# Kernel tuning notes

Hardware: AMD Instinct MI355X
Metric: run time of the kernel (lower is better)

Reference implementation:

```python
import jax, jax.numpy as jnp
import numpy as np

N_E, FEAT, REST = 2048, 512, 8
HEAD, LENGTH = 8, 64


def setup_inputs() -> dict:
    key = jax.random.key(0)
    kx, kq, kk, kd = jax.random.split(key, 4)
    x = jax.random.normal(kx, (N_E, FEAT, REST), dtype=jnp.float32)
    Q = jax.random.normal(kq, (HEAD, LENGTH, FEAT), dtype=jnp.float32)
    K = jax.random.normal(kk, (HEAD, LENGTH, FEAT), dtype=jnp.float32)
    D = jax.random.normal(kd, (HEAD, LENGTH, FEAT), dtype=jnp.float32)
    return {"x": x, "Q": Q, "K": K, "D": D}


def _linear(a, W):
    # a: (n, f, *rest), W: (h, q, f) -> y: (n, h, q, *rest)
    y = jnp.einsum('nf...,hqf->nhq...', a, W)
    # L2-normalize over the last 3 axes (here: h? no -- axes (q, rest...) per the
    # original code: sum over (-1,-2,-3) of (n,h,q,rest) = (h,q,rest) per n)
    norm = jnp.sqrt((y * y).sum((-1, -2, -3), keepdims=True))
    return y / norm


def reference(x, Q, K, D):
    n_e = x.shape[0]
    rest = x.shape[2:]
    head, length = Q.shape[0], Q.shape[1]
    q = _linear(x, Q)  # (n, h, l, rest)
    k = _linear(x, K)
    d = _linear(x, D)
    # scores over electrons: contract (l, rest) -> (h, n, n)
    w = jax.nn.softmax(jnp.einsum('nh...,mh...->hnm', q, k), axis=-1)
    # weighted combine: (h,n,m) x (m,h,l,rest) -> (n,h,l,rest)
    v = jnp.einsum('hnm,mhl...->nhl...', w, d)
    return v.reshape((n_e, head * length) + rest)
```

## Files before the change

kernel.cpp:

```cpp
#include <hip/hip_runtime.h>
#include <math.h>

#define NE   2048
#define FEAT 512

typedef short short8 __attribute__((ext_vector_type(8)));
typedef float f32x4  __attribute__((ext_vector_type(4)));

__device__ __forceinline__ unsigned short f2bf(float f) {
    union { float f; unsigned u; } v; v.f = f;
    unsigned r = v.u + 0x7fffu + ((v.u >> 16) & 1u);
    return (unsigned short)(r >> 16);
}
__device__ __forceinline__ float bf2f(unsigned b) {
    union { unsigned u; float f; } v; v.u = b << 16;
    return v.f;
}
__device__ __forceinline__ unsigned pack2(float a, float b) {
    return (unsigned)f2bf(a) | ((unsigned)f2bf(b) << 16);
}

__device__ __forceinline__ void gld16(unsigned short* lds, const unsigned short* g) {
    __builtin_amdgcn_global_load_lds(
        (const __attribute__((address_space(1))) unsigned int*)g,
        (__attribute__((address_space(3))) unsigned int*)lds,
        16, 0, 0);
}


__global__ __launch_bounds__(256) void wconv_kernel(
    const float* __restrict__ Wq, const float* __restrict__ Wk, const float* __restrict__ Wd,
    unsigned short* __restrict__ wbf)
{
    const int t = threadIdx.x;
    const float* W = (blockIdx.y == 0) ? Wq : (blockIdx.y == 1) ? Wk : Wd;
    unsigned short* o = wbf + (size_t)blockIdx.y * 262144;
    const int idx = blockIdx.x * 2048 + t * 8;
    const float4* p = (const float4*)(W + idx);
    float4 v0 = p[0], v1 = p[1];
    *(uint4*)(o + idx) = make_uint4(pack2(v0.x, v0.y), pack2(v0.z, v0.w),
                                    pack2(v1.x, v1.y), pack2(v1.z, v1.w));
}

__global__ __launch_bounds__(256) void xpose_kernel(const float* __restrict__ x,
                                                    unsigned short* __restrict__ xt)
{
    __shared__ float xs[8 * 516];
    const int t = threadIdx.x;
    const int n = blockIdx.x;
    const float4* xp = (const float4*)(x + (size_t)n * 4096);
    #pragma unroll
    for (int i = 0; i < 4; ++i) {
        int idx = t + 256 * i;
        float4 v = xp[idx];
        int f = idx >> 1, rh = (idx & 1) * 4;
        xs[(rh + 0) * 516 + f] = v.x;
        xs[(rh + 1) * 516 + f] = v.y;
        xs[(rh + 2) * 516 + f] = v.z;
        xs[(rh + 3) * 516 + f] = v.w;
    }
    __syncthreads();
    const int r = t >> 5, f0 = (t & 31) * 16;
    const float* src = &xs[r * 516 + f0];
    unsigned o[8];
    #pragma unroll
    for (int j = 0; j < 8; ++j) o[j] = pack2(src[2 * j], src[2 * j + 1]);
    unsigned short* dst = xt + (size_t)n * 4096 + r * 512 + f0;
    *(uint4*)dst       = make_uint4(o[0], o[1], o[2], o[3]);
    *(uint4*)(dst + 8) = make_uint4(o[4], o[5], o[6], o[7]);
}

__global__ __launch_bounds__(256) void proj_gemm(
    const unsigned short* __restrict__ wbf, const unsigned short* __restrict__ xt,
    unsigned short* __restrict__ qb, unsigned short* __restrict__ kb, unsigned short* __restrict__ db)
{
    __shared__ unsigned short SM[17408];
    const int t = threadIdx.x;
    const int w = blockIdx.z;
    const unsigned short* W = wbf + (size_t)w * 262144;
    unsigned short* out = (w == 0) ? qb : (w == 1) ? kb : db;
    const int M0 = blockIdx.y * 128;
    const int N0 = blockIdx.x * 128;
    const int wave = t >> 6, lane = t & 63, quad = lane >> 4, l16 = lane & 15;
    const int lrow = lane >> 3;
    const int scol = ((lane & 7) ^ lrow) * 8;
    unsigned short* As = SM;
    unsigned short* Bs = SM + 8192;

    f32x4 acc[2][8];
    #pragma unroll
    for (int i = 0; i < 2; ++i)
        #pragma unroll
        for (int j = 0; j < 8; ++j) acc[i][j] = {0.f, 0.f, 0.f, 0.f};

    for (int kc = 0; kc < 8; ++kc) {
        #pragma unroll
        for (int p = 0; p < 4; ++p) {
            int c = p * 4 + wave;
            gld16(As + c * 512, W  + (size_t)(M0 + c * 8 + lrow) * 512 + kc * 64 + scol);
            gld16(Bs + c * 512, xt + (size_t)(N0 + c * 8 + lrow) * 512 + kc * 64 + scol);
        }
        __syncthreads();
        #pragma unroll
        for (int kk = 0; kk < 2; ++kk) {
            int so = ((kk * 4 + quad) ^ (l16 & 7)) * 8;
            short8 a0 = *(const short8*)&As[(wave * 32 + l16) * 64 + so];
            short8 a1 = *(const short8*)&As[(wave * 32 + 16 + l16) * 64 + so];
            #pragma unroll
            for (int ct = 0; ct < 8; ++ct) {
                short8 bb = *(const short8*)&Bs[(ct * 16 + l16) * 64 + so];
                acc[0][ct] = __builtin_amdgcn_mfma_f32_16x16x32_bf16(a0, bb, acc[0][ct], 0, 0, 0);
                acc[1][ct] = __builtin_amdgcn_mfma_f32_16x16x32_bf16(a1, bb, acc[1][ct], 0, 0, 0);
            }
        }
        __syncthreads();
    }

    unsigned short* T = SM;
    #pragma unroll
    for (int rt = 0; rt < 2; ++rt)
        #pragma unroll
        for (int reg = 0; reg < 4; ++reg) {
            int row = wave * 32 + rt * 16 + quad * 4 + reg;
            #pragma unroll
            for (int ct = 0; ct < 8; ++ct)
                T[row * 136 + ct * 16 + l16] = f2bf(acc[rt][ct][reg]);
        }
    __syncthreads();
    #pragma unroll
    for (int i = 0; i < 8; ++i) {
        int c = t + 256 * i;
        int n = c >> 7, row = c & 127;
        uint4 v = *(const uint4*)(T + row * 136 + n * 8);
        int hl = M0 + row;
        unsigned short* dst = out + (size_t)(hl >> 6) * 1048576 + (size_t)(hl & 63) * 8
                                  + (size_t)((N0 >> 3) + n) * 512;
        *(uint4*)dst = v;
    }
}

__global__ __launch_bounds__(256) void scales_kernel(
    const unsigned short* __restrict__ qb, const unsigned short* __restrict__ kb,
    const unsigned short* __restrict__ db, float* __restrict__ scales)
{
    __shared__ float red[256];
    const int t = threadIdx.x;
    const int n = blockIdx.x, w = blockIdx.y;
    const unsigned short* src = (w == 0) ? qb : (w == 1) ? kb : db;
    const int h = t >> 5, f0 = (t & 31) * 16;
    const unsigned short* p = src + ((size_t)h * NE + n) * 512 + f0;
    uint4 v0 = *(const uint4*)p;
    uint4 v1 = *(const uint4*)(p + 8);
    unsigned a[8] = {v0.x, v0.y, v0.z, v0.w, v1.x, v1.y, v1.z, v1.w};
    float s = 0.f;
    #pragma unroll
    for (int j = 0; j < 8; ++j) {
        float lo = bf2f(a[j] & 0xffffu), hi = bf2f(a[j] >> 16);
        s += lo * lo + hi * hi;
    }
    red[t] = s;
    __syncthreads();
    for (int st = 128; st > 0; st >>= 1) {
        if (t < st) red[t] += red[t + st];
        __syncthreads();
    }
    if (t == 0) scales[w * NE + n] = rsqrtf(red[0]);
}

__global__ __launch_bounds__(256) void dtrans_kernel(
    const unsigned short* __restrict__ db, const float* __restrict__ invd,
    unsigned short* __restrict__ dT)
{
    __shared__ float Ts[64 * 68];
    const int t = threadIdx.x;
    const int h = blockIdx.z, n0 = blockIdx.y * 64, f0 = blockIdx.x * 64;
    const int rr = t >> 3, cs = (t & 7) * 8;
    #pragma unroll
    for (int p = 0; p < 2; ++p) {
        int row = rr + p * 32;
        float sc = invd[n0 + row];
        uint4 v = *(const uint4*)(db + ((size_t)h * NE + n0 + row) * 512 + f0 + cs);
        unsigned a[4] = {v.x, v.y, v.z, v.w};
        float* d = &Ts[row * 68 + cs];
        #pragma unroll
        for (int j = 0; j < 4; ++j) {
            d[2 * j]     = bf2f(a[j] & 0xffffu) * sc;
            d[2 * j + 1] = bf2f(a[j] >> 16) * sc;
        }
    }
    __syncthreads();
    const int f = t >> 2, ns = (t & 3) * 16;
    unsigned o[8];
    #pragma unroll
    for (int j = 0; j < 8; ++j)
        o[j] = pack2(Ts[(ns + 2 * j) * 68 + f], Ts[(ns + 2 * j + 1) * 68 + f]);
    unsigned short* dst = dT + ((size_t)h * 512 + f0 + f) * NE + n0 + ns;
    *(uint4*)dst       = make_uint4(o[0], o[1], o[2], o[3]);
    *(uint4*)(dst + 8) = make_uint4(o[4], o[5], o[6], o[7]);
}

__global__ __launch_bounds__(256) void score_kernel(
    const unsigned short* __restrict__ qb, const unsigned short* __restrict__ kb,
    const float* __restrict__ scales, unsigned short* __restrict__ P,
    float* __restrict__ sums, int g)
{
    __shared__ unsigned short As[8192];
    __shared__ unsigned short Bs[8192];
    const int t = threadIdx.x;
    int bid = blockIdx.x + 16 * (blockIdx.y + 16 * blockIdx.z);
    int swz = (bid & 7) * 128 + (bid >> 3);
    const int bx = swz & 15, by = (swz >> 4) & 15, bz = swz >> 8;
    const int hg = bz, h = g * 4 + hg;
    const int n0 = by * 128, m0 = bx * 128;
    const int wave = t >> 6, lane = t & 63, quad = lane >> 4, l16 = lane & 15;
    const int lrow = lane >> 3;
    const int scol = ((lane & 7) ^ lrow) * 8;
    const unsigned short* qh = qb + (size_t)h * NE * 512;
    const unsigned short* kh = kb + (size_t)h * NE * 512;

    f32x4 acc[2][8];
    #pragma unroll
    for (int i = 0; i < 2; ++i)
        #pragma unroll
        for (int j = 0; j < 8; ++j) acc[i][j] = {0.f, 0.f, 0.f, 0.f};

    for (int kc = 0; kc < 8; ++kc) {
        #pragma unroll
        for (int p = 0; p < 4; ++p) {
            int c = p * 4 + wave;
            gld16(As + c * 512, qh + (size_t)(n0 + c * 8 + lrow) * 512 + kc * 64 + scol);
            gld16(Bs + c * 512, kh + (size_t)(m0 + c * 8 + lrow) * 512 + kc * 64 + scol);
        }
        __syncthreads();
        #pragma unroll
        for (int kk = 0; kk < 2; ++kk) {
            int so = ((kk * 4 + quad) ^ (l16 & 7)) * 8;
            short8 a0 = *(const short8*)&As[(wave * 32 + l16) * 64 + so];
            short8 a1 = *(const short8*)&As[(wave * 32 + 16 + l16) * 64 + so];
            #pragma unroll
            for (int ct = 0; ct < 8; ++ct) {
                short8 bb = *(const short8*)&Bs[(ct * 16 + l16) * 64 + so];
                acc[0][ct] = __builtin_amdgcn_mfma_f32_16x16x32_bf16(a0, bb, acc[0][ct], 0, 0, 0);
                acc[1][ct] = __builtin_amdgcn_mfma_f32_16x16x32_bf16(a1, bb, acc[1][ct], 0, 0, 0);
            }
        }
        __syncthreads();
    }

    float iq[2][4], ik[8];
    #pragma unroll
    for (int rt = 0; rt < 2; ++rt)
        #pragma unroll
        for (int reg = 0; reg < 4; ++reg)
            iq[rt][reg] = scales[n0 + wave * 32 + rt * 16 + quad * 4 + reg];
    #pragma unroll
    for (int ct = 0; ct < 8; ++ct) ik[ct] = scales[NE + m0 + ct * 16 + l16];

    unsigned short* Ph = P + (size_t)hg * NE * NE;
    #pragma unroll
    for (int rt = 0; rt < 2; ++rt)
        #pragma unroll
        for (int reg = 0; reg < 4; ++reg) {
            int nl = wave * 32 + rt * 16 + quad * 4 + reg;
            unsigned short* prow = Ph + (size_t)(n0 + nl) * NE + m0;
            float qs = iq[rt][reg];
            float rs = 0.f;
            #pragma unroll
            for (int ct = 0; ct < 8; ++ct) {
                float e = __expf(acc[rt][ct][reg] * qs * ik[ct]);
                unsigned short bx16 = f2bf(e);
                prow[ct * 16 + l16] = bx16;
                rs += bf2f(bx16);
            }
            rs += __shfl_xor(rs, 1);
            rs += __shfl_xor(rs, 2);
            rs += __shfl_xor(rs, 4);
            rs += __shfl_xor(rs, 8);
            if (l16 == 0) atomicAdd(&sums[hg * NE + n0 + nl], rs);
        }
}

__global__ __launch_bounds__(512) void combine_kernel(
    const unsigned short* __restrict__ P, const unsigned short* __restrict__ dT,
    const float* __restrict__ sums, float* __restrict__ out, int g)
{
    __shared__ unsigned short Ps[8192];
    __shared__ unsigned short Ds[8192];
    const int t = threadIdx.x;
    int bid = blockIdx.x + 4 * (blockIdx.y + 16 * blockIdx.z);
    int swz = (bid & 7) * 32 + (bid >> 3);
    const int bx = swz & 3, by = (swz >> 2) & 15, bz = swz >> 6;
    const int hg = bz, h = g * 4 + hg;
    const int n0 = by * 128, f0 = bx * 128;
    const int wave = t >> 6, lane = t & 63, quad = lane >> 4, l16 = lane & 15;
    const int wn = wave >> 1, wf = wave & 1;
    const int lrow = lane >> 3;
    const int scol = ((lane & 7) ^ lrow) * 8;
    const unsigned short* Ph = P + (size_t)hg * NE * NE;
    const unsigned short* dh = dT + (size_t)h * 512 * NE;

    f32x4 acc[2][4];
    #pragma unroll
    for (int i = 0; i < 2; ++i)
        #pragma unroll
        for (int j = 0; j < 4; ++j) acc[i][j] = {0.f, 0.f, 0.f, 0.f};

    for (int mc = 0; mc < 32; ++mc) {
        #pragma unroll
        for (int p = 0; p < 2; ++p) {
            int c = p * 8 + wave;
            gld16(Ps + c * 512, Ph + (size_t)(n0 + c * 8 + lrow) * NE + mc * 64 + scol);
            gld16(Ds + c * 512, dh + (size_t)(f0 + c * 8 + lrow) * NE + mc * 64 + scol);
        }
        __syncthreads();
        #pragma unroll
        for (int kk = 0; kk < 2; ++kk) {
            int so = ((kk * 4 + quad) ^ (l16 & 7)) * 8;
            short8 a0 = *(const short8*)&Ps[(wn * 32 + l16) * 64 + so];
            short8 a1 = *(const short8*)&Ps[(wn * 32 + 16 + l16) * 64 + so];
            #pragma unroll
            for (int ct = 0; ct < 4; ++ct) {
                short8 bb = *(const short8*)&Ds[(wf * 64 + ct * 16 + l16) * 64 + so];
                acc[0][ct] = __builtin_amdgcn_mfma_f32_16x16x32_bf16(a0, bb, acc[0][ct], 0, 0, 0);
                acc[1][ct] = __builtin_amdgcn_mfma_f32_16x16x32_bf16(a1, bb, acc[1][ct], 0, 0, 0);
            }
        }
        __syncthreads();
    }

    #pragma unroll
    for (int rt = 0; rt < 2; ++rt)
        #pragma unroll
        for (int reg = 0; reg < 4; ++reg) {
            int nl = wn * 32 + rt * 16 + quad * 4 + reg;
            float li = 1.0f / sums[hg * NE + n0 + nl];
            float* orow = out + (size_t)(n0 + nl) * 4096 + h * 512 + f0 + wf * 64;
            #pragma unroll
            for (int ct = 0; ct < 4; ++ct)
                orow[ct * 16 + l16] = acc[rt][ct][reg] * li;
        }
}

extern "C" void kernel_launch(void* const* d_in, const int* in_sizes, int n_in,
                              void* d_out, int out_size, void* d_ws, size_t ws_size,
                              hipStream_t stream)
{
    const float* x  = (const float*)d_in[0];
    const float* Qw = (const float*)d_in[1];
    const float* Kw = (const float*)d_in[2];
    const float* Dw = (const float*)d_in[3];
    float* out = (float*)d_out;

    char* ws = (char*)d_ws;
    unsigned short* xt = (unsigned short*)ws;
    unsigned short* db = (unsigned short*)(ws + 16777216);
    unsigned short* P  = (unsigned short*)ws;
    unsigned short* qb = (unsigned short*)(ws + 33554432);
    unsigned short* kb = (unsigned short*)(ws + 33554432 + 16777216);
    unsigned short* dT = (unsigned short*)(ws + 33554432 + 2 * 16777216);
    unsigned short* wbf = dT;
    float* scales = (float*)(ws + 83886080);
    float* sums   = (float*)(ws + 83886080 + 24576);

    wconv_kernel<<<dim3(128, 3), 256, 0, stream>>>(Qw, Kw, Dw, wbf);
    xpose_kernel<<<2048, 256, 0, stream>>>(x, xt);
    proj_gemm<<<dim3(128, 4, 3), 256, 0, stream>>>(wbf, xt, qb, kb, db);
    scales_kernel<<<dim3(2048, 3), 256, 0, stream>>>(qb, kb, db, scales);
    dtrans_kernel<<<dim3(8, 32, 8), 256, 0, stream>>>(db, scales + 2 * NE, dT);
    for (int g = 0; g < 2; ++g) {
        hipMemsetAsync(sums, 0, 4 * NE * sizeof(float), stream);
        score_kernel<<<dim3(16, 16, 4), 256, 0, stream>>>(qb, kb, scales, P, sums, g);
        combine_kernel<<<dim3(4, 16, 4), 512, 0, stream>>>(P, dT, sums, out, g);
    }
}
```

Baseline: 271.1 us.

## Double-buffer LDS loads in score and combine kernels, enlarge score tiles

The score kernel moves from 128x128 tiles with 256 threads to 256x256 tiles with 512 threads. It uses a two-stage LDS double buffer with explicit vmcnt waits and raw barriers, so global-to-LDS loads for step k+2 overlap compute on step k. The combine kernel gets the same double-buffered prefetch scheme. Larger tiles raise data reuse per loaded byte, but use 128KB of LDS and many accumulator registers per block, which lowers occupancy and leaves fewer blocks (256) to fill the CUs.

```diff
diff --git a/kernel.cpp b/kernel.cpp
--- a/kernel.cpp
+++ b/kernel.cpp
@@ -26,6 +26,13 @@
         (__attribute__((address_space(3))) unsigned int*)lds,
         16, 0, 0);
 }
+
+__device__ __forceinline__ void bar() {
+    asm volatile("" ::: "memory");
+    __builtin_amdgcn_s_barrier();
+    asm volatile("" ::: "memory");
+}
+#define VMW(n) asm volatile("s_waitcnt vmcnt(" #n ")" ::: "memory")
 
 
 __global__ __launch_bounds__(256) void wconv_kernel(
@@ -199,84 +206,101 @@
     *(uint4*)(dst + 8) = make_uint4(o[4], o[5], o[6], o[7]);
 }
 
-__global__ __launch_bounds__(256) void score_kernel(
+__global__ __launch_bounds__(512, 2) void score_kernel(
     const unsigned short* __restrict__ qb, const unsigned short* __restrict__ kb,
     const float* __restrict__ scales, unsigned short* __restrict__ P,
     float* __restrict__ sums, int g)
 {
-    __shared__ unsigned short As[8192];
-    __shared__ unsigned short Bs[8192];
-    const int t = threadIdx.x;
-    int bid = blockIdx.x + 16 * (blockIdx.y + 16 * blockIdx.z);
-    int swz = (bid & 7) * 128 + (bid >> 3);
-    const int bx = swz & 15, by = (swz >> 4) & 15, bz = swz >> 8;
+    __shared__ unsigned short SM[65536];
+    const int t = threadIdx.x;
+    int bid = blockIdx.x + 8 * (blockIdx.y + 8 * blockIdx.z);
+    int swz = (bid & 7) * 32 + (bid >> 3);
+    const int bx = swz & 7, by = (swz >> 3) & 7, bz = swz >> 6;
     const int hg = bz, h = g * 4 + hg;
-    const int n0 = by * 128, m0 = bx * 128;
+    const int n0 = by * 256, m0 = bx * 256;
     const int wave = t >> 6, lane = t & 63, quad = lane >> 4, l16 = lane & 15;
+    const int wr = wave >> 2, wc = wave & 3;
     const int lrow = lane >> 3;
     const int scol = ((lane & 7) ^ lrow) * 8;
     const unsigned short* qh = qb + (size_t)h * NE * 512;
     const unsigned short* kh = kb + (size_t)h * NE * 512;
 
-    f32x4 acc[2][8];
-    #pragma unroll
-    for (int i = 0; i < 2; ++i)
-        #pragma unroll
-        for (int j = 0; j < 8; ++j) acc[i][j] = {0.f, 0.f, 0.f, 0.f};
-
-    for (int kc = 0; kc < 8; ++kc) {
+    f32x4 acc[8][4];
+    #pragma unroll
+    for (int m = 0; m < 8; ++m)
+        #pragma unroll
+        for (int n = 0; n < 4; ++n) acc[m][n] = {0.f, 0.f, 0.f, 0.f};
+
+    auto STAGE = [&](int kc, int buf) {
+        unsigned short* A = SM + buf * 16384;
+        unsigned short* B = SM + 32768 + buf * 16384;
         #pragma unroll
         for (int p = 0; p < 4; ++p) {
-            int c = p * 4 + wave;
-            gld16(As + c * 512, qh + (size_t)(n0 + c * 8 + lrow) * 512 + kc * 64 + scol);
-            gld16(Bs + c * 512, kh + (size_t)(m0 + c * 8 + lrow) * 512 + kc * 64 + scol);
-        }
-        __syncthreads();
+            int c = p * 8 + wave;
+            gld16(A + c * 512, qh + (size_t)(n0 + c * 8 + lrow) * 512 + kc * 64 + scol);
+        }
+        #pragma unroll
+        for (int p = 0; p < 4; ++p) {
+            int c = p * 8 + wave;
+            gld16(B + c * 512, kh + (size_t)(m0 + c * 8 + lrow) * 512 + kc * 64 + scol);
+        }
+    };
+    auto COMPUTE = [&](int buf) {
+        const unsigned short* A = SM + buf * 16384;
+        const unsigned short* B = SM + 32768 + buf * 16384;
         #pragma unroll
         for (int kk = 0; kk < 2; ++kk) {
             int so = ((kk * 4 + quad) ^ (l16 & 7)) * 8;
-            short8 a0 = *(const short8*)&As[(wave * 32 + l16) * 64 + so];
-            short8 a1 = *(const short8*)&As[(wave * 32 + 16 + l16) * 64 + so];
-            #pragma unroll
-            for (int ct = 0; ct < 8; ++ct) {
-                short8 bb = *(const short8*)&Bs[(ct * 16 + l16) * 64 + so];
-                acc[0][ct] = __builtin_amdgcn_mfma_f32_16x16x32_bf16(a0, bb, acc[0][ct], 0, 0, 0);
-                acc[1][ct] = __builtin_amdgcn_mfma_f32_16x16x32_bf16(a1, bb, acc[1][ct], 0, 0, 0);
-            }
-        }
-        __syncthreads();
-    }
-
-    float iq[2][4], ik[8];
-    #pragma unroll
-    for (int rt = 0; rt < 2; ++rt)
-        #pragma unroll
-        for (int reg = 0; reg < 4; ++reg)
-            iq[rt][reg] = scales[n0 + wave * 32 + rt * 16 + quad * 4 + reg];
-    #pragma unroll
-    for (int ct = 0; ct < 8; ++ct) ik[ct] = scales[NE + m0 + ct * 16 + l16];
+            short8 a[8], b[4];
+            #pragma unroll
+            for (int m = 0; m < 8; ++m)
+                a[m] = *(const short8*)&A[(wr * 128 + m * 16 + l16) * 64 + so];
+            #pragma unroll
+            for (int n = 0; n < 4; ++n)
+                b[n] = *(const short8*)&B[(wc * 64 + n * 16 + l16) * 64 + so];
+            #pragma unroll
+            for (int m = 0; m < 8; ++m)
+                #pragma unroll
+                for (int n = 0; n < 4; ++n)
+                    acc[m][n] = __builtin_amdgcn_mfma_f32_16x16x32_bf16(a[m], b[n], acc[m][n], 0, 0, 0);
+        }
+    };
+
+    STAGE(0, 0);
+    STAGE(1, 1);
+    for (int kc = 0; kc < 8; ++kc) {
+        if (kc < 7) { VMW(8); } else { VMW(0); }
+        bar();
+        COMPUTE(kc & 1);
+        bar();
+        if (kc + 2 < 8) STAGE(kc + 2, kc & 1);
+    }
+
+    float ik[4];
+    #pragma unroll
+    for (int n = 0; n < 4; ++n) ik[n] = scales[NE + m0 + wc * 64 + n * 16 + l16];
 
     unsigned short* Ph = P + (size_t)hg * NE * NE;
     #pragma unroll
-    for (int rt = 0; rt < 2; ++rt)
+    for (int m = 0; m < 8; ++m)
         #pragma unroll
         for (int reg = 0; reg < 4; ++reg) {
-            int nl = wave * 32 + rt * 16 + quad * 4 + reg;
-            unsigned short* prow = Ph + (size_t)(n0 + nl) * NE + m0;
-            float qs = iq[rt][reg];
+            int row = n0 + wr * 128 + m * 16 + quad * 4 + reg;
+            float qs = scales[row];
+            unsigned short* prow = Ph + (size_t)row * NE + m0 + wc * 64;
             float rs = 0.f;
             #pragma unroll
-            for (int ct = 0; ct < 8; ++ct) {
-                float e = __expf(acc[rt][ct][reg] * qs * ik[ct]);
+            for (int n = 0; n < 4; ++n) {
+                float e = __expf(acc[m][n][reg] * qs * ik[n]);
                 unsigned short bx16 = f2bf(e);
-                prow[ct * 16 + l16] = bx16;
+                prow[n * 16 + l16] = bx16;
                 rs += bf2f(bx16);
             }
             rs += __shfl_xor(rs, 1);
             rs += __shfl_xor(rs, 2);
             rs += __shfl_xor(rs, 4);
             rs += __shfl_xor(rs, 8);
-            if (l16 == 0) atomicAdd(&sums[hg * NE + n0 + nl], rs);
+            if (l16 == 0) atomicAdd(&sums[hg * NE + row], rs);
         }
 }
 
@@ -284,8 +308,8 @@
     const unsigned short* __restrict__ P, const unsigned short* __restrict__ dT,
     const float* __restrict__ sums, float* __restrict__ out, int g)
 {
-    __shared__ unsigned short Ps[8192];
-    __shared__ unsigned short Ds[8192];
+    __shared__ unsigned short Ps[2][8192];
+    __shared__ unsigned short Ds[2][8192];
     const int t = threadIdx.x;
     int bid = blockIdx.x + 4 * (blockIdx.y + 16 * blockIdx.z);
     int swz = (bid & 7) * 32 + (bid >> 3);
@@ -305,27 +329,37 @@
         #pragma unroll
         for (int j = 0; j < 4; ++j) acc[i][j] = {0.f, 0.f, 0.f, 0.f};
 
-    for (int mc = 0; mc < 32; ++mc) {
+    auto STAGE = [&](int mc, int buf) {
         #pragma unroll
         for (int p = 0; p < 2; ++p) {
             int c = p * 8 + wave;
-            gld16(Ps + c * 512, Ph + (size_t)(n0 + c * 8 + lrow) * NE + mc * 64 + scol);
-            gld16(Ds + c * 512, dh + (size_t)(f0 + c * 8 + lrow) * NE + mc * 64 + scol);
-        }
-        __syncthreads();
+            gld16(&Ps[buf][c * 512], Ph + (size_t)(n0 + c * 8 + lrow) * NE + mc * 64 + scol);
+            gld16(&Ds[buf][c * 512], dh + (size_t)(f0 + c * 8 + lrow) * NE + mc * 64 + scol);
+        }
+    };
+    auto COMPUTE = [&](int buf) {
         #pragma unroll
         for (int kk = 0; kk < 2; ++kk) {
             int so = ((kk * 4 + quad) ^ (l16 & 7)) * 8;
-            short8 a0 = *(const short8*)&Ps[(wn * 32 + l16) * 64 + so];
-            short8 a1 = *(const short8*)&Ps[(wn * 32 + 16 + l16) * 64 + so];
+            short8 a0 = *(const short8*)&Ps[buf][(wn * 32 + l16) * 64 + so];
+            short8 a1 = *(const short8*)&Ps[buf][(wn * 32 + 16 + l16) * 64 + so];
             #pragma unroll
             for (int ct = 0; ct < 4; ++ct) {
-                short8 bb = *(const short8*)&Ds[(wf * 64 + ct * 16 + l16) * 64 + so];
+                short8 bb = *(const short8*)&Ds[buf][(wf * 64 + ct * 16 + l16) * 64 + so];
                 acc[0][ct] = __builtin_amdgcn_mfma_f32_16x16x32_bf16(a0, bb, acc[0][ct], 0, 0, 0);
                 acc[1][ct] = __builtin_amdgcn_mfma_f32_16x16x32_bf16(a1, bb, acc[1][ct], 0, 0, 0);
             }
         }
-        __syncthreads();
+    };
+
+    STAGE(0, 0);
+    STAGE(1, 1);
+    for (int mc = 0; mc < 32; ++mc) {
+        if (mc < 31) { VMW(4); } else { VMW(0); }
+        bar();
+        COMPUTE(mc & 1);
+        bar();
+        if (mc + 2 < 32) STAGE(mc + 2, mc & 1);
     }
 
     #pragma unroll
@@ -369,7 +403,7 @@
     dtrans_kernel<<<dim3(8, 32, 8), 256, 0, stream>>>(db, scales + 2 * NE, dT);
     for (int g = 0; g < 2; ++g) {
         hipMemsetAsync(sums, 0, 4 * NE * sizeof(float), stream);
-        score_kernel<<<dim3(16, 16, 4), 256, 0, stream>>>(qb, kb, scales, P, sums, g);
+        score_kernel<<<dim3(8, 8, 4), 512, 0, stream>>>(qb, kb, scales, P, sums, g);
         combine_kernel<<<dim3(4, 16, 4), 512, 0, stream>>>(P, dT, sums, out, g);
     }
 }
```

After: 268.5 us. About the same (-1.0%).
